# Kernel optimization log

Measured on AMD Instinct MI355X. Metric: run time of the kernel, lower is better.

The kernel has to match this reference:

```python
import jax, jax.numpy as jnp
import numpy as np

K = 7  # kernel_size (odd)
PAD = K // 2
EPS = 1e-12  # F.normalize eps


def setup_inputs() -> dict:
    key = jax.random.key(0)
    kx, ky = jax.random.split(key)
    B, C, H, W = 4, 256, 256, 256
    x = jax.random.normal(kx, (B, C, H, W), dtype=jnp.float32)
    y = jax.random.normal(ky, (B, C, H, W), dtype=jnp.float32)
    return {"x": x, "y": y}


def _l2_normalize(t):
    # F.normalize(t, p=2, dim=1): divide by channel L2 norm, clamped at eps
    n = jnp.sqrt(jnp.sum(t * t, axis=1, keepdims=True))
    return t / jnp.maximum(n, EPS)


def reference(x, y):
    xn = _l2_normalize(x)
    yn = _l2_normalize(y)
    B, C, H, W = x.shape  # H == W assumed (module mixes h/w in slicing)
    yp = jnp.pad(yn, ((0, 0), (0, 0), (PAD, PAD), (PAD, PAD)))
    # Fixed K*K offset loop (small, static); each term reduces over channels.
    sims = [
        jnp.sum(xn * jax.lax.dynamic_slice(yp, (0, 0, i, j), (B, C, H, W)), axis=1)
        for i in range(K)
        for j in range(K)
    ]
    return jnp.stack(sims, axis=1)  # [B, K*K, H, W]
```

## Files before the change

kernel.cpp:

```cpp
#include <hip/hip_runtime.h>


#define H_ 256
#define W_ 256
#define C_ 256
#define B_ 4
#define TH 16
#define TW 16
#define KCH 32
#define NCHUNK (C_ / KCH)
#define HAL (TH + 6)
#define WAL (TW + 6)
#define YW 32
#define PLANE (H_ * W_)

typedef __attribute__((ext_vector_type(8))) short short8;
typedef __attribute__((ext_vector_type(4))) float floatx4;

__device__ __forceinline__ unsigned bfpair(float a, float b) {
  unsigned ua = __float_as_uint(a), ub = __float_as_uint(b);
  ua = (ua + 0x7FFFu + ((ua >> 16) & 1u)) >> 16;
  ub = (ub + 0x7FFFu + ((ub >> 16) & 1u)) & 0xFFFF0000u;
  return ub | ua;
}

__global__ __launch_bounds__(1024) void ncorr(const float* __restrict__ x,
                                              const float* __restrict__ y,
                                              float* __restrict__ out) {
  __shared__ short Yb[HAL * YW * KCH];
  __shared__ short Xb[TH * TW * KCH];
  __shared__ float sxl[TH * TW];
  __shared__ float syl[HAL * WAL];

  const int t = threadIdx.x;
  const int b = blockIdx.z;
  const int h0 = blockIdx.y * TH;
  const int w0 = blockIdx.x * TW;

  for (int idx = t; idx < HAL * 10 * (KCH / 2); idx += 1024) {
    int hy = idx / (10 * (KCH / 2));
    int r = idx - hy * (10 * (KCH / 2));
    int wy = 22 + r / (KCH / 2);
    int cp = r - (r / (KCH / 2)) * (KCH / 2);
    ((unsigned*)Yb)[((hy * YW + wy) * KCH) / 2 + cp] = 0u;
  }
  if (t < TH * TW) sxl[t] = 0.f;
  if (t < HAL * WAL) syl[t] = 0.f;

  int xidx[4], xlds[4];
  float sxacc[4];
#pragma unroll
  for (int i = 0; i < 4; i++) {
    int s = t + i * 1024;
    int cp = s >> 8;
    int h = (s >> 4) & 15;
    int w = s & 15;
    xidx[i] = ((b * C_ + 2 * cp) * H_ + (h0 + h)) * W_ + (w0 + w);
    xlds[i] = (h * TW + w) * KCH + 2 * cp;
    sxacc[i] = 0.f;
  }
  int yidx[8], ylds[8], ysl[8];
  float syacc[8];
  unsigned yok = 0;
#pragma unroll
  for (int i = 0; i < 8; i++) {
    int s = t + i * 1024;
    int cp = s / 484;
    int r = s - cp * 484;
    int hy = r / 22;
    int wy = r - hy * 22;
    int gy = h0 - 3 + hy;
    int gx = w0 - 3 + wy;
    bool inimg = (gy >= 0) && (gy < H_) && (gx >= 0) && (gx < W_);
    if (inimg) yok |= (1u << i);
    yidx[i] = ((b * C_ + 2 * cp) * H_ + (inimg ? gy : 0)) * W_ + (inimg ? gx : 0);
    ylds[i] = (hy * YW + wy) * KCH + 2 * cp;
    ysl[i] = r;
    syacc[i] = 0.f;
  }

  const int lane = t & 63;
  const int wv = t >> 6;
  const int q = lane >> 4;
  const int lr = lane & 15;

  floatx4 acc[7][2];
#pragma unroll
  for (int i = 0; i < 7; i++) {
    acc[i][0] = (floatx4){0.f, 0.f, 0.f, 0.f};
    acc[i][1] = (floatx4){0.f, 0.f, 0.f, 0.f};
  }

  for (int ch = 0; ch < NCHUNK; ch++) {
    __syncthreads();
    const int coff = ch * (KCH * PLANE);
#pragma unroll
    for (int i = 0; i < 4; i++) {
      const float* p = x + xidx[i] + coff;
      float f0 = p[0], f1 = p[PLANE];
      sxacc[i] += f0 * f0 + f1 * f1;
      *(unsigned*)&Xb[xlds[i]] = bfpair(f0, f1);
    }
#pragma unroll
    for (int i = 0; i < 8; i++) {
      if (i == 7 && t >= 576) break;
      float f0 = 0.f, f1 = 0.f;
      if ((yok >> i) & 1) {
        const float* p = y + yidx[i] + coff;
        f0 = p[0];
        f1 = p[PLANE];
      }
      syacc[i] += f0 * f0 + f1 * f1;
      *(unsigned*)&Yb[ylds[i]] = bfpair(f0, f1);
    }
    __syncthreads();
    short8 A = *(const short8*)&Xb[(wv * TW + lr) * KCH + q * 8];
#pragma unroll
    for (int i = 0; i < 7; i++) {
      const int hy = wv + i;
#pragma unroll
      for (int nt = 0; nt < 2; nt++) {
        short8 Bf = *(const short8*)&Yb[(hy * YW + nt * 16 + lr) * KCH + q * 8];
        acc[i][nt] = __builtin_amdgcn_mfma_f32_16x16x32_bf16(A, Bf, acc[i][nt], 0, 0, 0);
      }
    }
  }

  __syncthreads();
#pragma unroll
  for (int i = 0; i < 4; i++) atomicAdd(&sxl[(t + i * 1024) & 255], sxacc[i]);
#pragma unroll
  for (int i = 0; i < 8; i++) {
    if (i == 7 && t >= 576) break;
    atomicAdd(&syl[ysl[i]], syacc[i]);
  }
  __syncthreads();
  if (t < TH * TW) sxl[t] = 1.f / fmaxf(sqrtf(sxl[t]), 1e-12f);
  if (t < HAL * WAL) syl[t] = 1.f / fmaxf(sqrtf(syl[t]), 1e-12f);
  __syncthreads();

  const int h = wv;
#pragma unroll
  for (int i = 0; i < 7; i++) {
#pragma unroll
    for (int nt = 0; nt < 2; nt++) {
      const int n = nt * 16 + lr;
#pragma unroll
      for (int r = 0; r < 4; r++) {
        const int m = q * 4 + r;
        const int j = n - m;
        if (j >= 0 && j < 7) {
          float v = acc[i][nt][r] * sxl[h * TW + m] * syl[(h + i) * WAL + n];
          out[((b * 49 + 7 * i + j) * H_ + (h0 + h)) * W_ + (w0 + m)] = v;
        }
      }
    }
  }
}

extern "C" void kernel_launch(void* const* d_in, const int* in_sizes, int n_in,
                              void* d_out, int out_size, void* d_ws, size_t ws_size,
                              hipStream_t stream) {
  const float* x = (const float*)d_in[0];
  const float* y = (const float*)d_in[1];
  float* out = (float*)d_out;
  dim3 grid(W_ / TW, H_ / TH, B_);
  ncorr<<<grid, 1024, 0, stream>>>(x, y, out);
}
```

Measured before the change: 828.9 us.

## Halve tile height, load 8 channels per thread, stage outputs through LDS

Tile height drops from 16 to 8 and the block shrinks to 512 threads with a launch bound allowing more blocks per CU. Each thread now loads 8 channel values and writes a 16-byte packed bf16 vector to LDS, replacing 2-channel 4-byte stores. Outputs are staged in LDS and written back with a coalesced loop instead of scattered per-element stores. The cost is a larger y halo relative to the tile, so more redundant y reads per output, and an extra barrier and LDS pass at the end.

```diff
diff --git a/kernel.cpp b/kernel.cpp
--- a/kernel.cpp
+++ b/kernel.cpp
@@ -5,7 +5,7 @@
 #define W_ 256
 #define C_ 256
 #define B_ 4
-#define TH 16
+#define TH 8
 #define TW 16
 #define KCH 32
 #define NCHUNK (C_ / KCH)
@@ -13,9 +13,11 @@
 #define WAL (TW + 6)
 #define YW 32
 #define PLANE (H_ * W_)
+#define NYSLOT (HAL * WAL * 4)
 
 typedef __attribute__((ext_vector_type(8))) short short8;
 typedef __attribute__((ext_vector_type(4))) float floatx4;
+typedef __attribute__((ext_vector_type(4))) unsigned uintx4;
 
 __device__ __forceinline__ unsigned bfpair(float a, float b) {
   unsigned ua = __float_as_uint(a), ub = __float_as_uint(b);
@@ -24,65 +26,70 @@
   return ub | ua;
 }
 
-__global__ __launch_bounds__(1024) void ncorr(const float* __restrict__ x,
-                                              const float* __restrict__ y,
-                                              float* __restrict__ out) {
-  __shared__ short Yb[HAL * YW * KCH];
-  __shared__ short Xb[TH * TW * KCH];
+__device__ __forceinline__ uintx4 pack8(const float f[8]) {
+  uintx4 r;
+  r.x = bfpair(f[0], f[1]);
+  r.y = bfpair(f[2], f[3]);
+  r.z = bfpair(f[4], f[5]);
+  r.w = bfpair(f[6], f[7]);
+  return r;
+}
+
+__global__ __launch_bounds__(512, 8) void ncorr(const float* __restrict__ x,
+                                                const float* __restrict__ y,
+                                                float* __restrict__ out) {
+  __shared__ __align__(16) char ldsbuf[HAL * YW * KCH * 2 + TH * TW * KCH * 2];
   __shared__ float sxl[TH * TW];
   __shared__ float syl[HAL * WAL];
+  short* Yb = (short*)ldsbuf;
+  short* Xb = (short*)(ldsbuf + HAL * YW * KCH * 2);
+  float* Ot = (float*)ldsbuf;
 
   const int t = threadIdx.x;
+  const int lane = t & 63;
+  const int wv = t >> 6;
+  const int q = lane >> 4;
+  const int lr = lane & 15;
   const int b = blockIdx.z;
   const int h0 = blockIdx.y * TH;
   const int w0 = blockIdx.x * TW;
 
-  for (int idx = t; idx < HAL * 10 * (KCH / 2); idx += 1024) {
-    int hy = idx / (10 * (KCH / 2));
-    int r = idx - hy * (10 * (KCH / 2));
-    int wy = 22 + r / (KCH / 2);
-    int cp = r - (r / (KCH / 2)) * (KCH / 2);
-    ((unsigned*)Yb)[((hy * YW + wy) * KCH) / 2 + cp] = 0u;
+  for (int idx = t; idx < HAL * 10 * (KCH / 2); idx += 512) {
+    int hy = idx / 160;
+    int r = idx - hy * 160;
+    int wy = 22 + (r >> 4);
+    int dw = r & 15;
+    ((unsigned*)Yb)[(hy * YW + wy) * (KCH / 2) + dw] = 0u;
   }
   if (t < TH * TW) sxl[t] = 0.f;
   if (t < HAL * WAL) syl[t] = 0.f;
 
-  int xidx[4], xlds[4];
-  float sxacc[4];
+  const int xcg = lane & 3;
+  const int xw = (lane >> 2) & 15;
+  const int xgidx = ((b * C_ + xcg * 8) * H_ + (h0 + wv)) * W_ + (w0 + xw);
+  const int xlds = (wv * TW + xw) * KCH + xcg * 8;
+  float sxacc = 0.f;
+
+  int yidx[3], ylds[3], ypos[3];
+  unsigned yval = 0, yok = 0;
+  float syacc[3] = {0.f, 0.f, 0.f};
 #pragma unroll
-  for (int i = 0; i < 4; i++) {
-    int s = t + i * 1024;
-    int cp = s >> 8;
-    int h = (s >> 4) & 15;
-    int w = s & 15;
-    xidx[i] = ((b * C_ + 2 * cp) * H_ + (h0 + h)) * W_ + (w0 + w);
-    xlds[i] = (h * TW + w) * KCH + 2 * cp;
-    sxacc[i] = 0.f;
-  }
-  int yidx[8], ylds[8], ysl[8];
-  float syacc[8];
-  unsigned yok = 0;
-#pragma unroll
-  for (int i = 0; i < 8; i++) {
-    int s = t + i * 1024;
-    int cp = s / 484;
-    int r = s - cp * 484;
-    int hy = r / 22;
-    int wy = r - hy * 22;
+  for (int i = 0; i < 3; i++) {
+    int s = t + i * 512;
+    bool valid = s < NYSLOT;
+    int cg = s & 3;
+    int p = s >> 2;
+    int hy = p / WAL;
+    int wy = p - hy * WAL;
     int gy = h0 - 3 + hy;
     int gx = w0 - 3 + wy;
-    bool inimg = (gy >= 0) && (gy < H_) && (gx >= 0) && (gx < W_);
+    bool inimg = valid && gy >= 0 && gy < H_ && gx >= 0 && gx < W_;
+    if (valid) yval |= (1u << i);
     if (inimg) yok |= (1u << i);
-    yidx[i] = ((b * C_ + 2 * cp) * H_ + (inimg ? gy : 0)) * W_ + (inimg ? gx : 0);
-    ylds[i] = (hy * YW + wy) * KCH + 2 * cp;
-    ysl[i] = r;
-    syacc[i] = 0.f;
+    yidx[i] = ((b * C_ + cg * 8) * H_ + (inimg ? gy : 0)) * W_ + (inimg ? gx : 0);
+    ylds[i] = (hy * YW + wy) * KCH + cg * 8;
+    ypos[i] = p;
   }
-
-  const int lane = t & 63;
-  const int wv = t >> 6;
-  const int q = lane >> 4;
-  const int lr = lane & 15;
 
   floatx4 acc[7][2];
 #pragma unroll
@@ -94,52 +101,50 @@
   for (int ch = 0; ch < NCHUNK; ch++) {
     __syncthreads();
     const int coff = ch * (KCH * PLANE);
+    {
+      const float* p = x + xgidx + coff;
+      float f[8];
 #pragma unroll
-    for (int i = 0; i < 4; i++) {
-      const float* p = x + xidx[i] + coff;
-      float f0 = p[0], f1 = p[PLANE];
-      sxacc[i] += f0 * f0 + f1 * f1;
-      *(unsigned*)&Xb[xlds[i]] = bfpair(f0, f1);
+      for (int k = 0; k < 8; k++) f[k] = p[k * PLANE];
+#pragma unroll
+      for (int k = 0; k < 8; k++) sxacc += f[k] * f[k];
+      *(uintx4*)&Xb[xlds] = pack8(f);
     }
 #pragma unroll
-    for (int i = 0; i < 8; i++) {
-      if (i == 7 && t >= 576) break;
-      float f0 = 0.f, f1 = 0.f;
+    for (int i = 0; i < 3; i++) {
+      if (!((yval >> i) & 1)) continue;
+      float f[8] = {0.f, 0.f, 0.f, 0.f, 0.f, 0.f, 0.f, 0.f};
       if ((yok >> i) & 1) {
         const float* p = y + yidx[i] + coff;
-        f0 = p[0];
-        f1 = p[PLANE];
+#pragma unroll
+        for (int k = 0; k < 8; k++) f[k] = p[k * PLANE];
       }
-      syacc[i] += f0 * f0 + f1 * f1;
-      *(unsigned*)&Yb[ylds[i]] = bfpair(f0, f1);
+#pragma unroll
+      for (int k = 0; k < 8; k++) syacc[i] += f[k] * f[k];
+      *(uintx4*)&Yb[ylds[i]] = pack8(f);
     }
     __syncthreads();
     short8 A = *(const short8*)&Xb[(wv * TW + lr) * KCH + q * 8];
 #pragma unroll
     for (int i = 0; i < 7; i++) {
-      const int hy = wv + i;
 #pragma unroll
       for (int nt = 0; nt < 2; nt++) {
-        short8 Bf = *(const short8*)&Yb[(hy * YW + nt * 16 + lr) * KCH + q * 8];
+        short8 Bf = *(const short8*)&Yb[((wv + i) * YW + nt * 16 + lr) * KCH + q * 8];
         acc[i][nt] = __builtin_amdgcn_mfma_f32_16x16x32_bf16(A, Bf, acc[i][nt], 0, 0, 0);
       }
     }
   }
 
   __syncthreads();
+  atomicAdd(&sxl[wv * TW + xw], sxacc);
 #pragma unroll
-  for (int i = 0; i < 4; i++) atomicAdd(&sxl[(t + i * 1024) & 255], sxacc[i]);
-#pragma unroll
-  for (int i = 0; i < 8; i++) {
-    if (i == 7 && t >= 576) break;
-    atomicAdd(&syl[ysl[i]], syacc[i]);
-  }
+  for (int i = 0; i < 3; i++)
+    if ((yval >> i) & 1) atomicAdd(&syl[ypos[i]], syacc[i]);
   __syncthreads();
   if (t < TH * TW) sxl[t] = 1.f / fmaxf(sqrtf(sxl[t]), 1e-12f);
   if (t < HAL * WAL) syl[t] = 1.f / fmaxf(sqrtf(syl[t]), 1e-12f);
   __syncthreads();
 
-  const int h = wv;
 #pragma unroll
   for (int i = 0; i < 7; i++) {
 #pragma unroll
@@ -150,11 +155,19 @@
         const int m = q * 4 + r;
         const int j = n - m;
         if (j >= 0 && j < 7) {
-          float v = acc[i][nt][r] * sxl[h * TW + m] * syl[(h + i) * WAL + n];
-          out[((b * 49 + 7 * i + j) * H_ + (h0 + h)) * W_ + (w0 + m)] = v;
+          Ot[(7 * i + j) * (TH * TW) + wv * TW + m] =
+              acc[i][nt][r] * sxl[wv * TW + m] * syl[(wv + i) * WAL + n];
         }
       }
     }
+  }
+  __syncthreads();
+  for (int idx = t; idx < 49 * TH * TW; idx += 512) {
+    int p = idx >> 7;
+    int rem = idx & 127;
+    int hh = rem >> 4;
+    int ww = rem & 15;
+    out[((b * 49 + p) * H_ + (h0 + hh)) * W_ + (w0 + ww)] = Ot[idx];
   }
 }
 
@@ -165,5 +178,5 @@
   const float* y = (const float*)d_in[1];
   float* out = (float*)d_out;
   dim3 grid(W_ / TW, H_ / TH, B_);
-  ncorr<<<grid, 1024, 0, stream>>>(x, y, out);
+  ncorr<<<grid, 512, 0, stream>>>(x, y, out);
 }
```

Result: slower. 1.262 ms (+52.2%).
